# Optimization experiments

Measured on AMD Instinct MI355X. Metric: run time of the kernel, lower is better.

The kernel has to match this reference:

```python
import jax, jax.numpy as jnp
import numpy as np

D_MODEL = 1024
NUM_HEADS = 16
HEAD_DIM = D_MODEL // NUM_HEADS


def setup_inputs() -> dict:
    key = jax.random.key(0)
    ks = jax.random.split(key, 5)
    B, S = 4, 2048
    scale = 0.02
    return {
        "x": jax.random.normal(ks[0], (B, S, D_MODEL), dtype=jnp.float32),
        "q_proj_weight": jax.random.normal(ks[1], (D_MODEL, D_MODEL), dtype=jnp.float32) * scale,
        "k_proj_weight": jax.random.normal(ks[2], (D_MODEL, D_MODEL), dtype=jnp.float32) * scale,
        "v_proj_weight": jax.random.normal(ks[3], (D_MODEL, D_MODEL), dtype=jnp.float32) * scale,
        "o_proj_weight": jax.random.normal(ks[4], (D_MODEL, D_MODEL), dtype=jnp.float32) * scale,
    }


def reference(x, q_proj_weight, k_proj_weight, v_proj_weight, o_proj_weight):
    B, S, _ = x.shape
    H, Dh = NUM_HEADS, HEAD_DIM

    def proj(w):  # [B,S,d_model] x [d_k,d_in] -> [B,H,S,Dh]
        p = jnp.einsum('bsd,kd->bsk', x, w)
        return p.reshape(B, S, H, Dh).transpose(0, 2, 1, 3)

    q = proj(q_proj_weight)
    k = proj(k_proj_weight)
    v = proj(v_proj_weight)

    scores = jnp.einsum('bhqd,bhkd->bhqk', q, k) / jnp.sqrt(jnp.asarray(Dh, dtype=x.dtype))
    causal = jnp.tril(jnp.ones((S, S), dtype=bool))  # [S,S]
    scores = jnp.where(causal, scores, -jnp.inf)
    attn = jax.nn.softmax(scores, axis=-1)
    out = jnp.einsum('bhqk,bhkd->bhqd', attn, v)  # [B,H,S,Dh]
    out = out.transpose(0, 2, 1, 3).reshape(B, S, D_MODEL)
    return jnp.einsum('bsv,mv->bsm', out, o_proj_weight)
```

## Files before the change

kernel.cpp:

```cpp
#include <hip/hip_runtime.h>
#include <cstdint>
#include <cstddef>

#define NH 16
#define DH 64
#define SEQ 2048
#define DM 1024

typedef __attribute__((ext_vector_type(8))) short short8;
typedef __attribute__((ext_vector_type(4))) float f32x4;

__device__ __forceinline__ unsigned short f2bf(float f) {
  unsigned u = __builtin_bit_cast(unsigned, f);
  u += 0x7fffu + ((u >> 16) & 1u);
  return (unsigned short)(u >> 16);
}

__device__ __forceinline__ void gld_lds16(const void* g, void* l) {
  __builtin_amdgcn_global_load_lds((const __attribute__((address_space(1))) void*)g,
                                   (__attribute__((address_space(3))) void*)l,
                                   16, 0, 0);
}

__global__ __launch_bounds__(256) void cast_all_kernel(const float* __restrict__ x,
                                                       const float* __restrict__ wq,
                                                       const float* __restrict__ wk,
                                                       const float* __restrict__ wv,
                                                       const float* __restrict__ wo,
                                                       unsigned short* __restrict__ xb,
                                                       unsigned short* __restrict__ wqkvb,
                                                       unsigned short* __restrict__ wob) {
  const int bid = blockIdx.x;
  const float* in;
  unsigned short* out;
  int i;
  if (bid < 8192) {
    in = x; out = xb; i = bid * 256 + threadIdx.x;
  } else {
    const int w = (bid - 8192) >> 10;
    i = ((bid - 8192) & 1023) * 256 + threadIdx.x;
    in = (w == 0) ? wq : (w == 1) ? wk : (w == 2) ? wv : wo;
    out = (w < 3) ? (wqkvb + (size_t)w * 1048576) : wob;
  }
  const float4 v = ((const float4*)in)[i];
  ushort4 o;
  o.x = f2bf(v.x); o.y = f2bf(v.y); o.z = f2bf(v.z); o.w = f2bf(v.w);
  ((ushort4*)out)[i] = o;
}

__global__ __launch_bounds__(512, 2) void gemm_qkv256(const unsigned short* __restrict__ A,
                                                      const unsigned short* __restrict__ W,
                                                      unsigned short* __restrict__ qb,
                                                      unsigned short* __restrict__ kb,
                                                      unsigned short* __restrict__ vtb) {
  extern __shared__ __align__(16) unsigned short smem[];
  unsigned short* As = smem;
  unsigned short* Bs = smem + 4 * 8192;

  const int t = threadIdx.x;
  const int lane = t & 63;
  const int wave = t >> 6;
  const int quad = lane >> 4;
  const int l16 = lane & 15;
  const int wm = (wave >> 2) * 128;
  const int wn = (wave & 3) * 64;

  const int bid = blockIdx.x;
  const int xcd = bid & 7;
  const int idx = bid >> 3;
  const int bm = (xcd * 4 + idx / 12) * 256;
  const int bn = (idx % 12) * 256;
  const int sel = bn >> 10;
  const int bnl = bn & 1023;

  f32x4 acc[8][4];
#pragma unroll
  for (int i = 0; i < 8; ++i)
#pragma unroll
    for (int j = 0; j < 4; ++j) acc[i][j] = {0.0f, 0.0f, 0.0f, 0.0f};

  const int r0 = t >> 2;
  const int c0 = (((t & 3) ^ ((r0 >> 1) & 3)) * 8);
  const unsigned short* Ag0 = A + (size_t)(bm + r0) * DM + c0;
  const unsigned short* Ag1 = A + (size_t)(bm + r0 + 128) * DM + c0;
  const unsigned short* Bg0 = W + (size_t)(bn + r0) * DM + c0;
  const unsigned short* Bg1 = W + (size_t)(bn + r0 + 128) * DM + c0;

#define STAGE_A(tt)                                                  \
  {                                                                  \
    unsigned short* d = As + ((tt) & 3) * 8192 + t * 8;              \
    gld_lds16(Ag0 + (tt) * 32, d);                                   \
    gld_lds16(Ag1 + (tt) * 32, d + 4096);                            \
  }
#define STAGE_B(tt)                                                  \
  {                                                                  \
    unsigned short* d = Bs + ((tt) & 3) * 8192 + t * 8;              \
    gld_lds16(Bg0 + (tt) * 32, d);                                   \
    gld_lds16(Bg1 + (tt) * 32, d + 4096);                            \
  }

  const int swz = (l16 >> 1) & 3;
  const int aoff = l16 * 32 + ((quad ^ swz) * 8);

#define QKV_TILE(tt, DO_STAGE)                                                             \
  {                                                                                        \
    const unsigned short* Ab = As + ((tt) & 3) * 8192;                                     \
    const unsigned short* Bb = Bs + ((tt) & 3) * 8192;                                     \
    short8 af[4], bfr[4];                                                                  \
    _Pragma("unroll")                                                                      \
    for (int i = 0; i < 4; ++i)                                                            \
      af[i] = *(const short8*)(Ab + (wm + i * 16) * 32 + aoff);                            \
    _Pragma("unroll")                                                                      \
    for (int j = 0; j < 4; ++j)                                                            \
      bfr[j] = *(const short8*)(Bb + (wn + j * 16) * 32 + aoff);                           \
    if (DO_STAGE) { STAGE_A((tt) + 3); }                                                   \
    __builtin_amdgcn_s_setprio(1);                                                         \
    _Pragma("unroll")                                                                      \
    for (int i = 0; i < 4; ++i)                                                            \
      _Pragma("unroll")                                                                    \
      for (int j = 0; j < 4; ++j)                                                          \
        acc[i][j] = __builtin_amdgcn_mfma_f32_16x16x32_bf16(af[i], bfr[j], acc[i][j], 0, 0, 0); \
    __builtin_amdgcn_s_setprio(0);                                                         \
    _Pragma("unroll")                                                                      \
    for (int i = 0; i < 4; ++i)                                                            \
      af[i] = *(const short8*)(Ab + (wm + 64 + i * 16) * 32 + aoff);                       \
    if (DO_STAGE) { STAGE_B((tt) + 3); }                                                   \
    __builtin_amdgcn_s_setprio(1);                                                         \
    _Pragma("unroll")                                                                      \
    for (int i = 0; i < 4; ++i)                                                            \
      _Pragma("unroll")                                                                    \
      for (int j = 0; j < 4; ++j)                                                          \
        acc[4 + i][j] = __builtin_amdgcn_mfma_f32_16x16x32_bf16(af[i], bfr[j], acc[4 + i][j], 0, 0, 0); \
    __builtin_amdgcn_s_setprio(0);                                                         \
  }

  STAGE_A(0); STAGE_B(0);
  STAGE_A(1); STAGE_B(1);
  STAGE_A(2); STAGE_B(2);

#pragma unroll 1
  for (int tt = 0; tt < 30; ++tt) {
    asm volatile("s_waitcnt vmcnt(8)" ::: "memory");
    __builtin_amdgcn_s_barrier();
    asm volatile("" ::: "memory");
    QKV_TILE(tt, tt < 29);
  }
  asm volatile("s_waitcnt vmcnt(4)" ::: "memory");
  __builtin_amdgcn_s_barrier();
  asm volatile("" ::: "memory");
  QKV_TILE(30, false);
  asm volatile("s_waitcnt vmcnt(0)" ::: "memory");
  __builtin_amdgcn_s_barrier();
  asm volatile("" ::: "memory");
  QKV_TILE(31, false);

#undef QKV_TILE
#undef STAGE_A
#undef STAGE_B

#pragma unroll
  for (int i = 0; i < 8; ++i) {
#pragma unroll
    for (int j = 0; j < 4; ++j) {
#pragma unroll
      for (int r = 0; r < 4; ++r) {
        const int m = bm + wm + i * 16 + quad * 4 + r;
        const int n = bnl + wn + j * 16 + l16;
        const float v = acc[i][j][r];
        if (sel == 0) {
          qb[(size_t)m * DM + n] = f2bf(v * 0.125f);
        } else if (sel == 1) {
          kb[(size_t)m * DM + n] = f2bf(v);
        } else {
          const int bb = m >> 11, s = m & 2047;
          const int h = n >> 6, d = n & 63;
          vtb[((size_t)((bb * NH + h) * DH + d)) * SEQ + s] = f2bf(v);
        }
      }
    }
  }
}

__global__ __launch_bounds__(256, 4) void gemm_o(const unsigned short* __restrict__ A,
                                                 const unsigned short* __restrict__ B,
                                                 float* __restrict__ C) {
  __shared__ __align__(16) unsigned short As[128 * 32];
  __shared__ __align__(16) unsigned short Bs[128 * 32];
  const int t = threadIdx.x;
  const int lane = t & 63;
  const int wave = t >> 6;
  const int quad = lane >> 4;
  const int l16 = lane & 15;
  const int wm = (wave >> 1) * 64;
  const int wn = (wave & 1) * 64;

  const int lid = blockIdx.x + 8 * blockIdx.y;
  const int xcd = lid & 7;
  const int idx = lid >> 3;
  const int bm = (xcd * 8 + idx / 8) * 128;
  const int bn = (idx % 8) * 128;

  f32x4 acc[4][4];
#pragma unroll
  for (int i = 0; i < 4; ++i)
#pragma unroll
    for (int j = 0; j < 4; ++j) acc[i][j] = {0.0f, 0.0f, 0.0f, 0.0f};

  const int srow = t >> 2;
  const int sc = (t & 3) ^ ((srow >> 1) & 3);
  const unsigned short* Ag1 = A + (size_t)(bm + srow) * DM + sc * 8;
  const unsigned short* Ag2 = A + (size_t)(bm + srow + 64) * DM + sc * 8;
  const unsigned short* Bg1 = B + (size_t)(bn + srow) * DM + sc * 8;
  const unsigned short* Bg2 = B + (size_t)(bn + srow + 64) * DM + sc * 8;
  const int swz = (l16 >> 1) & 3;

  for (int k0 = 0; k0 < DM; k0 += 32) {
    __syncthreads();
    gld_lds16(Ag1 + k0, As + t * 8);
    gld_lds16(Ag2 + k0, As + t * 8 + 2048);
    gld_lds16(Bg1 + k0, Bs + t * 8);
    gld_lds16(Bg2 + k0, Bs + t * 8 + 2048);
    __syncthreads();
    short8 af[4], bfr[4];
#pragma unroll
    for (int i = 0; i < 4; ++i)
      af[i] = *(const short8*)(As + (wm + i * 16 + l16) * 32 + ((quad ^ swz) * 8));
#pragma unroll
    for (int j = 0; j < 4; ++j)
      bfr[j] = *(const short8*)(Bs + (wn + j * 16 + l16) * 32 + ((quad ^ swz) * 8));
#pragma unroll
    for (int i = 0; i < 4; ++i)
#pragma unroll
      for (int j = 0; j < 4; ++j)
        acc[i][j] = __builtin_amdgcn_mfma_f32_16x16x32_bf16(af[i], bfr[j], acc[i][j], 0, 0, 0);
  }

#pragma unroll
  for (int i = 0; i < 4; ++i)
#pragma unroll
    for (int j = 0; j < 4; ++j)
#pragma unroll
      for (int r = 0; r < 4; ++r) {
        const int m = bm + wm + i * 16 + quad * 4 + r;
        const int n = bn + wn + j * 16 + l16;
        C[(size_t)m * DM + n] = acc[i][j][r];
      }
}

__global__ __launch_bounds__(512) void attn_kernel(const unsigned short* __restrict__ Q,
                                                   const unsigned short* __restrict__ K,
                                                   const unsigned short* __restrict__ Vt,
                                                   unsigned short* __restrict__ O) {
  __shared__ __align__(16) unsigned short Ks[128 * 64];
  __shared__ __align__(16) unsigned short Vs[64 * 128];
  __shared__ __align__(16) unsigned short Ps[8][16 * 136];
  const int t = threadIdx.x;
  const int lane = t & 63;
  const int wave = t >> 6;
  const int quad = lane >> 4;
  const int l16 = lane & 15;
  const int h = blockIdx.y;
  const int b = blockIdx.z;

  const int ksr1 = t >> 3;
  const int ksr2 = (t + 512) >> 3;
  const int koff1 = (b * SEQ + ksr1) * DM + h * 64 + (((t & 7) ^ (ksr1 & 7)) * 8);
  const int koff2 = (b * SEQ + ksr2) * DM + h * 64 + (((t & 7) ^ (ksr2 & 7)) * 8);
  const int vsr1 = t >> 4;
  const int vsr2 = (t + 512) >> 4;
  const int voff1 = ((b * NH + h) * DH + vsr1) * SEQ + (((t & 15) ^ (vsr1 & 15)) * 8);
  const int voff2 = ((b * NH + h) * DH + vsr2) * SEQ + (((t & 15) ^ (vsr2 & 15)) * 8);
  unsigned short* Pw = &Ps[wave][0];
  const int swz = l16 & 7;

#pragma unroll 1
  for (int pass = 0; pass < 2; ++pass) {
    const int qt = (pass == 0) ? (int)blockIdx.x : 15 - (int)blockIdx.x;
    const int qtile = qt * 128;
    const int row_lo = qtile + wave * 16;
    const int row_hi = row_lo + 15;

    const unsigned short* Qrow =
        Q + ((size_t)(b * SEQ + row_lo + l16)) * DM + h * 64;
    const short8 qf0 = *(const short8*)(Qrow + quad * 8);
    const short8 qf1 = *(const short8*)(Qrow + 32 + quad * 8);

    f32x4 o_acc[4];
#pragma unroll
    for (int nb = 0; nb < 4; ++nb) o_acc[nb] = {0.0f, 0.0f, 0.0f, 0.0f};
    float l_r[4] = {0.0f, 0.0f, 0.0f, 0.0f};

    const int ktiles = qt + 1;
    for (int kt = 0; kt < ktiles; ++kt) {
      const int kbase = kt * 128;
      __syncthreads();
      gld_lds16(K + koff1 + (size_t)kbase * DM, Ks + t * 8);
      gld_lds16(K + koff2 + (size_t)kbase * DM, Ks + (t + 512) * 8);
      gld_lds16(Vt + voff1 + kbase, Vs + t * 8);
      gld_lds16(Vt + voff2 + kbase, Vs + (t + 512) * 8);
      __syncthreads();

      if (kbase <= row_hi) {
        f32x4 s_acc[8];
#pragma unroll
        for (int nb = 0; nb < 8; ++nb) {
          s_acc[nb] = {0.0f, 0.0f, 0.0f, 0.0f};
          const short8 kf0 = *(const short8*)(Ks + (nb * 16 + l16) * 64 + ((quad ^ swz) * 8));
          const short8 kf1 = *(const short8*)(Ks + (nb * 16 + l16) * 64 + (((4 | quad) ^ swz) * 8));
          s_acc[nb] = __builtin_amdgcn_mfma_f32_16x16x32_bf16(qf0, kf0, s_acc[nb], 0, 0, 0);
          s_acc[nb] = __builtin_amdgcn_mfma_f32_16x16x32_bf16(qf1, kf1, s_acc[nb], 0, 0, 0);
        }

        const bool need_mask = (kbase + 127 > row_lo);
#pragma unroll
        for (int r = 0; r < 4; ++r) {
          const int qr = row_lo + quad * 4 + r;
#pragma unroll
          for (int nb = 0; nb < 8; ++nb) {
            float p = __expf(s_acc[nb][r]);
            if (need_mask) p = ((kbase + nb * 16 + l16) <= qr) ? p : 0.0f;
            l_r[r] += p;
            const unsigned u = __builtin_bit_cast(unsigned, p);
            Pw[(quad * 4 + r) * 136 + nb * 16 + l16] =
                (unsigned short)((u + 0x8000u) >> 16);
          }
        }

#pragma unroll
        for (int kk = 0; kk < 4; ++kk) {
          const short8 pf = *(const short8*)(Pw + l16 * 136 + kk * 32 + quad * 8);
#pragma unroll
          for (int nb = 0; nb < 4; ++nb) {
            const short8 vf = *(const short8*)(Vs + (nb * 16 + l16) * 128 +
                                               (((kk * 4 + quad) ^ l16) * 8));
            o_acc[nb] = __builtin_amdgcn_mfma_f32_16x16x32_bf16(pf, vf, o_acc[nb], 0, 0, 0);
          }
        }
      }
    }

#pragma unroll
    for (int r = 0; r < 4; ++r) {
      float ls = l_r[r];
      ls += __shfl_xor(ls, 1);
      ls += __shfl_xor(ls, 2);
      ls += __shfl_xor(ls, 4);
      ls += __shfl_xor(ls, 8);
      const float inv_l = 1.0f / ls;
      const int qr = row_lo + quad * 4 + r;
#pragma unroll
      for (int nb = 0; nb < 4; ++nb)
        O[((size_t)(b * SEQ + qr)) * DM + h * 64 + nb * 16 + l16] =
            f2bf(o_acc[nb][r] * inv_l);
    }
  }
}

extern "C" void kernel_launch(void* const* d_in, const int* in_sizes, int n_in,
                              void* d_out, int out_size, void* d_ws, size_t ws_size,
                              hipStream_t stream) {
  const float* x  = (const float*)d_in[0];
  const float* wq = (const float*)d_in[1];
  const float* wk = (const float*)d_in[2];
  const float* wv = (const float*)d_in[3];
  const float* wo = (const float*)d_in[4];

  char* ws = (char*)d_ws;
  unsigned short* xb    = (unsigned short*)(ws);
  unsigned short* wqkvb = (unsigned short*)(ws + 16777216);
  unsigned short* wob   = (unsigned short*)(ws + 23068672);
  unsigned short* qb    = (unsigned short*)(ws + 25165824);
  unsigned short* kb    = (unsigned short*)(ws + 41943040);
  unsigned short* vtb   = (unsigned short*)(ws + 58720256);
  unsigned short* aob   = (unsigned short*)(ws + 75497472);

  static bool s_attr_done = false;
  if (!s_attr_done) {
    hipFuncSetAttribute(reinterpret_cast<const void*>(gemm_qkv256),
                        hipFuncAttributeMaxDynamicSharedMemorySize, 131072);
    s_attr_done = true;
  }

  cast_all_kernel<<<12288, 256, 0, stream>>>(x, wq, wk, wv, wo, xb, wqkvb, wob);

  gemm_qkv256<<<dim3(384), dim3(512), 131072, stream>>>(xb, wqkvb, qb, kb, vtb);

  attn_kernel<<<dim3(8, NH, 4), 512, 0, stream>>>(qb, kb, vtb, aob);

  gemm_o<<<dim3(8, 64), 256, 0, stream>>>(aob, wob, (float*)d_out);
}
```

Before: 276.0 us.

## Restructure QKV GEMM into double-buffered 64-wide K tiles with phased barriers

The QKV projection GEMM changes from a 4-stage ring of 32-wide K tiles to a 2-buffer scheme with 64-wide K tiles and a new XOR swizzle on 128-byte LDS rows. Each tile is split into four MFMA sub-phases with barriers between them, and global-to-LDS loads for the next A and B halves are interleaved across those sub-phases. The aim is to halve the loop iterations, overlap loads with MFMA work more evenly, and cut LDS bank conflicts. In exchange it adds many more barriers per tile and keeps less prefetch depth in flight.

```diff
diff --git a/kernel.cpp b/kernel.cpp
--- a/kernel.cpp
+++ b/kernel.cpp
@@ -53,17 +53,15 @@
                                                       unsigned short* __restrict__ qb,
                                                       unsigned short* __restrict__ kb,
                                                       unsigned short* __restrict__ vtb) {
-  extern __shared__ __align__(16) unsigned short smem[];
-  unsigned short* As = smem;
-  unsigned short* Bs = smem + 4 * 8192;
+  extern __shared__ __align__(16) char sm[];
 
   const int t = threadIdx.x;
   const int lane = t & 63;
   const int wave = t >> 6;
   const int quad = lane >> 4;
   const int l16 = lane & 15;
-  const int wm = (wave >> 2) * 128;
-  const int wn = (wave & 3) * 64;
+  const int wr = wave >> 2;
+  const int wc = wave & 3;
 
   const int bid = blockIdx.x;
   const int xcd = bid & 7;
@@ -79,84 +77,130 @@
 #pragma unroll
     for (int j = 0; j < 4; ++j) acc[i][j] = {0.0f, 0.0f, 0.0f, 0.0f};
 
-  const int r0 = t >> 2;
-  const int c0 = (((t & 3) ^ ((r0 >> 1) & 3)) * 8);
-  const unsigned short* Ag0 = A + (size_t)(bm + r0) * DM + c0;
-  const unsigned short* Ag1 = A + (size_t)(bm + r0 + 128) * DM + c0;
-  const unsigned short* Bg0 = W + (size_t)(bn + r0) * DM + c0;
-  const unsigned short* Bg1 = W + (size_t)(bn + r0 + 128) * DM + c0;
-
-#define STAGE_A(tt)                                                  \
-  {                                                                  \
-    unsigned short* d = As + ((tt) & 3) * 8192 + t * 8;              \
-    gld_lds16(Ag0 + (tt) * 32, d);                                   \
-    gld_lds16(Ag1 + (tt) * 32, d + 4096);                            \
-  }
-#define STAGE_B(tt)                                                  \
-  {                                                                  \
-    unsigned short* d = Bs + ((tt) & 3) * 8192 + t * 8;              \
-    gld_lds16(Bg0 + (tt) * 32, d);                                   \
-    gld_lds16(Bg1 + (tt) * 32, d + 4096);                            \
-  }
-
-  const int swz = (l16 >> 1) & 3;
-  const int aoff = l16 * 32 + ((quad ^ swz) * 8);
-
-#define QKV_TILE(tt, DO_STAGE)                                                             \
+  const int r0s = t >> 3;
+  const int g0 = (((t & 7) ^ (r0s & 7)) * 8);
+  const unsigned short* aS0 = A + (size_t)(bm + r0s) * DM + g0;
+  const unsigned short* aS1 = A + (size_t)(bm + 64 + r0s) * DM + g0;
+  const unsigned short* bS0 = W + (size_t)(bn + r0s) * DM + g0;
+  const unsigned short* bS1 = W + (size_t)(bn + 64 + r0s) * DM + g0;
+  const int t16 = t * 16;
+
+  const int aswz = (quad ^ (l16 & 7)) * 16;
+  const int aRd0 = (wr * 128 + l16) * 128 + aswz;
+  const int aRd1 = aRd0 ^ 64;
+  const int bRd0 = 65536 + (wc * 64 + l16) * 128 + aswz;
+  const int bRd1 = bRd0 ^ 64;
+
+#define ST_A(U, TK, PAR)                                                                   \
   {                                                                                        \
-    const unsigned short* Ab = As + ((tt) & 3) * 8192;                                     \
-    const unsigned short* Bb = Bs + ((tt) & 3) * 8192;                                     \
-    short8 af[4], bfr[4];                                                                  \
+    gld_lds16(aS0 + (size_t)(U) * 131072 + (TK) * 64, sm + (PAR) * 32768 + (U) * 16384 + t16); \
+    gld_lds16(aS1 + (size_t)(U) * 131072 + (TK) * 64,                                      \
+              sm + (PAR) * 32768 + (U) * 16384 + 8192 + t16);                              \
+  }
+#define ST_B(U, TK, PAR)                                                                   \
+  {                                                                                        \
+    gld_lds16(bS0 + (size_t)(U) * 131072 + (TK) * 64,                                      \
+              sm + 65536 + (PAR) * 32768 + (U) * 16384 + t16);                             \
+    gld_lds16(bS1 + (size_t)(U) * 131072 + (TK) * 64,                                      \
+              sm + 65536 + (PAR) * 32768 + (U) * 16384 + 8192 + t16);                      \
+  }
+
+#define MM(AF, BF, IB, JB)                                                                 \
+  _Pragma("unroll")                                                                        \
+  for (int i = 0; i < 4; ++i)                                                              \
     _Pragma("unroll")                                                                      \
-    for (int i = 0; i < 4; ++i)                                                            \
-      af[i] = *(const short8*)(Ab + (wm + i * 16) * 32 + aoff);                            \
+    for (int j = 0; j < 2; ++j) {                                                          \
+      acc[(IB) + i][(JB) + j] = __builtin_amdgcn_mfma_f32_16x16x32_bf16(                   \
+          AF[i][0], BF[j][0], acc[(IB) + i][(JB) + j], 0, 0, 0);                           \
+      acc[(IB) + i][(JB) + j] = __builtin_amdgcn_mfma_f32_16x16x32_bf16(                   \
+          AF[i][1], BF[j][1], acc[(IB) + i][(JB) + j], 0, 0, 0);                           \
+    }
+
+#define TILE(T, PAR, SB, SA, VM)                                                           \
+  {                                                                                        \
+    short8 af0[4][2], af1[4][2], bf0[2][2], bf1[2][2];                                     \
+                                          \
     _Pragma("unroll")                                                                      \
-    for (int j = 0; j < 4; ++j)                                                            \
-      bfr[j] = *(const short8*)(Bb + (wn + j * 16) * 32 + aoff);                           \
-    if (DO_STAGE) { STAGE_A((tt) + 3); }                                                   \
+    for (int i = 0; i < 4; ++i) {                                                          \
+      af0[i][0] = *(const short8*)(sm + (PAR) * 32768 + i * 2048 + aRd0);                  \
+      af0[i][1] = *(const short8*)(sm + (PAR) * 32768 + i * 2048 + aRd1);                  \
+    }                                                                                      \
+    _Pragma("unroll")                                                                      \
+    for (int j = 0; j < 2; ++j) {                                                          \
+      bf0[j][0] = *(const short8*)(sm + (PAR) * 32768 + j * 2048 + bRd0);                  \
+      bf0[j][1] = *(const short8*)(sm + (PAR) * 32768 + j * 2048 + bRd1);                  \
+    }                                                                                      \
+    if (SB) ST_B(0, (T) + 1, (PAR) ^ 1);                                                   \
+    asm volatile("" ::: "memory");                                                         \
+    __builtin_amdgcn_s_barrier();                                                          \
+    asm volatile("s_waitcnt lgkmcnt(0)" ::: "memory");                                     \
     __builtin_amdgcn_s_setprio(1);                                                         \
+    MM(af0, bf0, 0, 0);                                                                    \
+    __builtin_amdgcn_s_setprio(0);                                                         \
+    asm volatile("" ::: "memory");                                                         \
+    __builtin_amdgcn_s_barrier();                                                          \
+                                                     \
     _Pragma("unroll")                                                                      \
-    for (int i = 0; i < 4; ++i)                                                            \
-      _Pragma("unroll")                                                                    \
-      for (int j = 0; j < 4; ++j)                                                          \
-        acc[i][j] = __builtin_amdgcn_mfma_f32_16x16x32_bf16(af[i], bfr[j], acc[i][j], 0, 0, 0); \
+    for (int i = 0; i < 4; ++i) {                                                          \
+      af1[i][0] = *(const short8*)(sm + (PAR) * 32768 + 8192 + i * 2048 + aRd0);           \
+      af1[i][1] = *(const short8*)(sm + (PAR) * 32768 + 8192 + i * 2048 + aRd1);           \
+    }                                                                                      \
+    if (SB) ST_B(1, (T) + 1, (PAR) ^ 1);                                                   \
+    asm volatile("" ::: "memory");                                                         \
+    __builtin_amdgcn_s_barrier();                                                          \
+    asm volatile("s_waitcnt lgkmcnt(0)" ::: "memory");                                     \
+    __builtin_amdgcn_s_setprio(1);                                                         \
+    MM(af1, bf0, 4, 0);                                                                    \
     __builtin_amdgcn_s_setprio(0);                                                         \
+    asm volatile("" ::: "memory");                                                         \
+    __builtin_amdgcn_s_barrier();                                                          \
+                  \
     _Pragma("unroll")                                                                      \
-    for (int i = 0; i < 4; ++i)                                                            \
-      af[i] = *(const short8*)(Ab + (wm + 64 + i * 16) * 32 + aoff);                       \
-    if (DO_STAGE) { STAGE_B((tt) + 3); }                                                   \
+    for (int j = 0; j < 2; ++j) {                                                          \
+      bf1[j][0] = *(const short8*)(sm + (PAR) * 32768 + (2 + j) * 2048 + bRd0);            \
+      bf1[j][1] = *(const short8*)(sm + (PAR) * 32768 + (2 + j) * 2048 + bRd1);            \
+    }                                                                                      \
+    if (SA) ST_A(0, (T) + 2, (PAR));                                                       \
+    asm volatile("" ::: "memory");                                                         \
+    __builtin_amdgcn_s_barrier();                                                          \
+    asm volatile("s_waitcnt lgkmcnt(0)" ::: "memory");                                     \
     __builtin_amdgcn_s_setprio(1);                                                         \
-    _Pragma("unroll")                                                                      \
-    for (int i = 0; i < 4; ++i)                                                            \
-      _Pragma("unroll")                                                                    \
-      for (int j = 0; j < 4; ++j)                                                          \
-        acc[4 + i][j] = __builtin_amdgcn_mfma_f32_16x16x32_bf16(af[i], bfr[j], acc[4 + i][j], 0, 0, 0); \
+    MM(af1, bf1, 4, 2);                                                                    \
     __builtin_amdgcn_s_setprio(0);                                                         \
-  }
-
-  STAGE_A(0); STAGE_B(0);
-  STAGE_A(1); STAGE_B(1);
-  STAGE_A(2); STAGE_B(2);
-
-#pragma unroll 1
-  for (int tt = 0; tt < 30; ++tt) {
-    asm volatile("s_waitcnt vmcnt(8)" ::: "memory");
-    __builtin_amdgcn_s_barrier();
-    asm volatile("" ::: "memory");
-    QKV_TILE(tt, tt < 29);
-  }
+    asm volatile("" ::: "memory");                                                         \
+    __builtin_amdgcn_s_barrier();                                                          \
+               \
+    if (SA) ST_A(1, (T) + 2, (PAR));                                                       \
+    asm volatile("" ::: "memory");                                                         \
+    __builtin_amdgcn_s_barrier();                                                          \
+    __builtin_amdgcn_s_setprio(1);                                                         \
+    MM(af0, bf1, 0, 2);                                                                    \
+    __builtin_amdgcn_s_setprio(0);                                                         \
+    if ((VM) == 4) asm volatile("s_waitcnt vmcnt(4)" ::: "memory");                        \
+    else if ((VM) == 0) asm volatile("s_waitcnt vmcnt(0)" ::: "memory");                   \
+    asm volatile("" ::: "memory");                                                         \
+    __builtin_amdgcn_s_barrier();                                                          \
+  }
+
+  ST_A(0, 0, 0); ST_A(1, 0, 0);
+  ST_B(0, 0, 0); ST_B(1, 0, 0);
+  ST_A(0, 1, 1); ST_A(1, 1, 1);
   asm volatile("s_waitcnt vmcnt(4)" ::: "memory");
   __builtin_amdgcn_s_barrier();
-  asm volatile("" ::: "memory");
-  QKV_TILE(30, false);
-  asm volatile("s_waitcnt vmcnt(0)" ::: "memory");
-  __builtin_amdgcn_s_barrier();
-  asm volatile("" ::: "memory");
-  QKV_TILE(31, false);
-
-#undef QKV_TILE
-#undef STAGE_A
-#undef STAGE_B
+
+#pragma unroll 1
+  for (int tp = 0; tp < 7; ++tp) {
+    const int T0 = tp * 2;
+    TILE(T0, 0, 1, 1, 4)
+    TILE(T0 + 1, 1, 1, 1, 4)
+  }
+  TILE(14, 0, 1, 0, 0)
+  TILE(15, 1, 0, 0, -1)
+
+#undef TILE
+#undef MM
+#undef ST_A
+#undef ST_B
 
 #pragma unroll
   for (int i = 0; i < 8; ++i) {
@@ -164,8 +208,8 @@
     for (int j = 0; j < 4; ++j) {
 #pragma unroll
       for (int r = 0; r < 4; ++r) {
-        const int m = bm + wm + i * 16 + quad * 4 + r;
-        const int n = bnl + wn + j * 16 + l16;
+        const int m = bm + wr * 128 + i * 16 + quad * 4 + r;
+        const int n = bnl + wc * 64 + j * 16 + l16;
         const float v = acc[i][j][r];
         if (sel == 0) {
           qb[(size_t)m * DM + n] = f2bf(v * 0.125f);
```

Result: faster. 268.5 us (-2.7%).
